# Kernel tuning notes

Hardware: AMD Instinct MI355X
Metric: run time of the kernel (lower is better)

The kernel has to match this reference:

```python
import math
import jax, jax.numpy as jnp
import numpy as np

EMB_DIM = 1024
CFG_N_HEADS = 16
# Faithful to the torch module: n_heads collapses to 1 when config.n_heads < emb_dim
N_HEADS = CFG_N_HEADS if CFG_N_HEADS >= EMB_DIM else 1


def setup_inputs() -> dict:
    key = jax.random.key(0)
    ks = jax.random.split(key, 11)
    B, T, C = 4, 2048, EMB_DIM
    s = 1.0 / math.sqrt(C)
    return {
        "q": jax.random.normal(ks[0], (B, T, C), jnp.float32),
        "k": jax.random.normal(ks[1], (B, T, C), jnp.float32),
        "v": jax.random.normal(ks[2], (B, T, C), jnp.float32),
        "Wq": jax.random.normal(ks[3], (C, C), jnp.float32) * s,
        "bq": jax.random.normal(ks[4], (C,), jnp.float32) * s,
        "Wk": jax.random.normal(ks[5], (C, C), jnp.float32) * s,
        "bk": jax.random.normal(ks[6], (C,), jnp.float32) * s,
        "Wv": jax.random.normal(ks[7], (C, C), jnp.float32) * s,
        "bv": jax.random.normal(ks[8], (C,), jnp.float32) * s,
        "Wff": jax.random.normal(ks[9], (C, C), jnp.float32) * s,
        "bff": jax.random.normal(ks[10], (C,), jnp.float32) * s,
    }


def reference(q, k, v, Wq, bq, Wk, bk, Wv, bv, Wff, bff):
    B, T, C = q.shape
    H = N_HEADS
    D = C // H  # head dim (== C here since H degenerates to 1)
    # torch Linear: x @ W.T + b
    qp = (q @ Wq.T + bq).reshape(B, T, H, D).transpose(0, 2, 1, 3)  # [B,H,T,D]
    kp = (k @ Wk.T + bk).reshape(B, T, H, D).transpose(0, 2, 1, 3)
    vp = (v @ Wv.T + bv).reshape(B, T, H, D).transpose(0, 2, 1, 3)
    scale = 1.0 / math.sqrt(D)
    scores = jnp.einsum('bhqd,bhkd->bhqk', qp, kp) * scale  # [B,H,T,T]
    causal = jnp.tril(jnp.ones((T, T), dtype=bool))
    scores = jnp.where(causal[None, None, :, :], scores, -jnp.inf)
    attn = jax.nn.softmax(scores, axis=-1)
    out = jnp.einsum('bhqk,bhkd->bhqd', attn, vp)  # [B,H,T,D]
    out = out.transpose(0, 2, 1, 3).reshape(B, T, C)
    return out @ Wff.T + bff
```

## Files before the change

kernel.cpp:

```cpp
#include <hip/hip_runtime.h>
#include <stdint.h>

typedef unsigned short u16;
typedef short v8s __attribute__((ext_vector_type(8)));
typedef short s4 __attribute__((ext_vector_type(4)));
typedef float v4f __attribute__((ext_vector_type(4)));

#define BM 128
#define BN 128
#define BK 64

__device__ __forceinline__ float b2f(u16 b) {
  union { unsigned u; float f; } x; x.u = ((unsigned)b) << 16; return x.f;
}
__device__ __forceinline__ u16 f2b(float f) {
  union { float f; unsigned u; } x; x.f = f;
  unsigned r = x.u + 0x7fffu + ((x.u >> 16) & 1u);
  return (u16)(r >> 16);
}

__device__ __forceinline__ void async_copy16(const void* g, void* lds) {
  __builtin_amdgcn_global_load_lds(
      (const __attribute__((address_space(1))) void*)g,
      (__attribute__((address_space(3))) void*)(uint32_t)(uintptr_t)lds,
      16, 0, 0);
}

__device__ __forceinline__ void xcd_swz(int& bx, int& by) {
  const int gx = gridDim.x;
  const int nwg = gx * gridDim.y;
  const int ord = blockIdx.y * gx + blockIdx.x;
  const int q = nwg >> 3, r = nwg & 7;
  const int xcd = ord & 7, local = ord >> 3;
  const int base = xcd < r ? xcd * (q + 1) : r * (q + 1) + (xcd - r) * q;
  const int s = base + local;
  bx = s % gx;
  by = s / gx;
}

__device__ __forceinline__ void causal_pair_swz(int& bx, int& by) {
  const int gx = gridDim.x;
  const int ord = blockIdx.y * gx + blockIdx.x;
  const int k = ord & 7;
  const int j = ord >> 3;
  by = (j < gx) ? k : 15 - k;
  bx = (j < gx) ? j : j - gx;
}

__global__ __launch_bounds__(256) void cvt_all_kernel(
    const float* __restrict__ i0, const float* __restrict__ i1,
    const float* __restrict__ i2, const float* __restrict__ i3,
    const float* __restrict__ i4, const float* __restrict__ i5,
    const float* __restrict__ i6, u16* __restrict__ o0, u16* __restrict__ o1,
    u16* __restrict__ o2, u16* __restrict__ o3, u16* __restrict__ o4,
    u16* __restrict__ o5, u16* __restrict__ o6, u16* __restrict__ o7,
    int n_big, int n_small, int n_l) {
  const int z = blockIdx.y;
  const int i = (blockIdx.x * 256 + threadIdx.x) * 8;
  if (z == 7) {
    if (i < n_l) *(v8s*)(o7 + i) = v8s{0, 0, 0, 0, 0, 0, 0, 0};
    return;
  }
  const float* in;
  u16* out;
  int n;
  switch (z) {
    case 0: in = i0; out = o0; n = n_big; break;
    case 1: in = i1; out = o1; n = n_big; break;
    case 2: in = i2; out = o2; n = n_big; break;
    case 3: in = i3; out = o3; n = n_small; break;
    case 4: in = i4; out = o4; n = n_small; break;
    case 5: in = i5; out = o5; n = n_small; break;
    default: in = i6; out = o6; n = n_small; break;
  }
  if (i >= n) return;
  v4f a = *(const v4f*)(in + i);
  v4f b = *(const v4f*)(in + i + 4);
  v8s o;
#pragma unroll
  for (int j = 0; j < 4; j++) o[j] = (short)f2b(a[j]);
#pragma unroll
  for (int j = 0; j < 4; j++) o[4 + j] = (short)f2b(b[j]);
  *(v8s*)(out + i) = o;
}

struct LdsS { u16 a[BM * BK]; u16 b[BN * BK]; };
union LdsU {
  LdsS s;
  u16 t[128 * 136];
};

template <bool HAS_BIAS, bool CAUSAL_K, bool OUT_F32, bool TR_OUT,
          bool EXP_OUT, bool NORM_L>
__device__ __forceinline__ void gemm_body(
    u16* ldsA, u16* ldsB, u16* ldsT, const u16* __restrict__ A, int lda,
    const u16* __restrict__ Bm, int ldb, void* __restrict__ Cout_, int ldc,
    long cbase, const float* __restrict__ bias, float* __restrict__ lsum,
    int K, int m0, int n0) {
  const int tid = threadIdx.x;
  const int wave = tid >> 6, lane = tid & 63;
  const int wm = (wave >> 1) * 64, wn = (wave & 1) * 64;
  const int lrow = lane & 15, quad = lane >> 4;

  v4f acc[4][4];
#pragma unroll
  for (int i = 0; i < 4; i++)
#pragma unroll
    for (int j = 0; j < 4; j++) acc[i][j] = v4f{0.f, 0.f, 0.f, 0.f};

  int Keff = K;
  if (CAUSAL_K) {
    int ke = m0 + BM;
    Keff = ke < K ? ke : K;
  }

  const int rA = lane >> 3;
  const int uch = (lane & 7) ^ rA;
  const u16* pA = A + (long)(m0 + wave * 8 + rA) * lda + uch * 8;
  const u16* pB = Bm + (long)(n0 + wave * 8 + rA) * ldb + uch * 8;
  u16* dA = ldsA + (wave * 8) * BK;
  u16* dB = ldsB + (wave * 8) * BK;

  for (int k0 = 0; k0 < Keff; k0 += BK) {
#pragma unroll
    for (int c = 0; c < 4; c++) {
      async_copy16(pA + (long)c * 32 * lda + k0, dA + c * 32 * BK);
      async_copy16(pB + (long)c * 32 * ldb + k0, dB + c * 32 * BK);
    }
    __syncthreads();

#pragma unroll
    for (int ks = 0; ks < 2; ks++) {
      v8s af[4], bfr[4];
#pragma unroll
      for (int mt = 0; mt < 4; mt++) {
        const int r = wm + mt * 16 + lrow;
        af[mt] =
            *(const v8s*)&ldsA[r * BK + ((ks * 4 + quad) ^ (r & 7)) * 8];
      }
#pragma unroll
      for (int nt = 0; nt < 4; nt++) {
        const int r = wn + nt * 16 + lrow;
        bfr[nt] =
            *(const v8s*)&ldsB[r * BK + ((ks * 4 + quad) ^ (r & 7)) * 8];
      }
#pragma unroll
      for (int mt = 0; mt < 4; mt++)
#pragma unroll
        for (int nt = 0; nt < 4; nt++)
          acc[mt][nt] = __builtin_amdgcn_mfma_f32_16x16x32_bf16(
              af[mt], bfr[nt], acc[mt][nt], 0, 0, 0);
    }
    __syncthreads();
  }

  if (TR_OUT) {
#pragma unroll
    for (int mt = 0; mt < 4; mt++) {
      const int rl = wm + mt * 16 + quad * 4;
#pragma unroll
      for (int nt = 0; nt < 4; nt++) {
        const int cl = wn + nt * 16 + lrow;
        float bv = 0.f;
        if (HAS_BIAS) bv = bias[n0 + cl];
        s4 w;
#pragma unroll
        for (int i = 0; i < 4; i++) w[i] = (short)f2b(acc[mt][nt][i] + bv);
        *(s4*)&ldsT[cl * 136 + rl] = w;
      }
    }
    __syncthreads();
    const int cl2 = tid >> 1, th = (tid & 1) * 64;
    const long bbase =
        (long)(m0 >> 11) * ((long)1024 * 2048) + (long)(m0 & 2047);
    u16* dst = (u16*)Cout_ + bbase + (long)(n0 + cl2) * 2048 + th;
    const u16* srcl = &ldsT[cl2 * 136 + th];
#pragma unroll
    for (int j = 0; j < 8; j++)
      *(v8s*)(dst + j * 8) = *(const v8s*)(srcl + j * 8);
    return;
  }

  if (EXP_OUT) {
    const float scale = 0.03125f;
#pragma unroll
    for (int mt = 0; mt < 4; mt++) {
      const int rowBase = m0 + wm + mt * 16 + quad * 4;
#pragma unroll
      for (int i = 0; i < 4; i++) {
        const int row = rowBase + i;
        float part = 0.f;
#pragma unroll
        for (int nt = 0; nt < 4; nt++) {
          const int col = n0 + wn + nt * 16 + lrow;
          float e = 0.f;
          if (col <= row) e = __expf(acc[mt][nt][i] * scale);
          part += e;
          ((u16*)Cout_)[cbase + (long)row * ldc + col] = f2b(e);
        }
        part += __shfl_xor(part, 1);
        part += __shfl_xor(part, 2);
        part += __shfl_xor(part, 4);
        part += __shfl_xor(part, 8);
        if (lrow == 0) atomicAdd(&lsum[row], part);
      }
    }
    return;
  }

  if (NORM_L) {
#pragma unroll
    for (int mt = 0; mt < 4; mt++) {
      const int rowBase = m0 + wm + mt * 16 + quad * 4;
#pragma unroll
      for (int i = 0; i < 4; i++) {
        const float inv = 1.0f / lsum[rowBase + i];
#pragma unroll
        for (int nt = 0; nt < 4; nt++) {
          const int col = n0 + wn + nt * 16 + lrow;
          ((u16*)Cout_)[cbase + (long)(rowBase + i) * ldc + col] =
              f2b(acc[mt][nt][i] * inv);
        }
      }
    }
    return;
  }

#pragma unroll
  for (int mt = 0; mt < 4; mt++) {
    const int rowBase = m0 + wm + mt * 16 + quad * 4;
#pragma unroll
    for (int nt = 0; nt < 4; nt++) {
      const int col = n0 + wn + nt * 16 + lrow;
      float bv = 0.f;
      if (HAS_BIAS) bv = bias[col];
#pragma unroll
      for (int i = 0; i < 4; i++) {
        const long idx = cbase + (long)(rowBase + i) * ldc + col;
        const float val = acc[mt][nt][i] + bv;
        if (OUT_F32)
          ((float*)Cout_)[idx] = val;
        else
          ((u16*)Cout_)[idx] = f2b(val);
      }
    }
  }
}

__global__ __launch_bounds__(256, 4) void qkv_gemm_kernel(
    const u16* __restrict__ a0, const u16* __restrict__ a1,
    const u16* __restrict__ a2, const u16* __restrict__ w0,
    const u16* __restrict__ w1, const u16* __restrict__ w2,
    const float* __restrict__ b0, const float* __restrict__ b1,
    const float* __restrict__ b2, u16* __restrict__ c0, u16* __restrict__ c1,
    u16* __restrict__ c2, int C) {
  __shared__ LdsU lds;
  const int z = blockIdx.z;
  const u16* A = z == 0 ? a0 : (z == 1 ? a1 : a2);
  const u16* W = z == 0 ? w0 : (z == 1 ? w1 : w2);
  const float* bias = z == 0 ? b0 : (z == 1 ? b1 : b2);
  u16* Cp = z == 0 ? c0 : (z == 1 ? c1 : c2);
  int bx, by;
  xcd_swz(bx, by);
  if (z == 2)
    gemm_body<true, false, false, true, false, false>(
        lds.s.a, lds.s.b, lds.t, A, C, W, C, Cp, C, 0, bias, nullptr, C,
        by * BM, bx * BN);
  else
    gemm_body<true, false, false, false, false, false>(
        lds.s.a, lds.s.b, nullptr, A, C, W, C, Cp, C, 0, bias, nullptr, C,
        by * BM, bx * BN);
}

template <bool HAS_BIAS, bool CAUSAL_SKIP, bool CAUSAL_K, bool OUT_F32,
          int SWZ, bool EXP_OUT, bool NORM_L>
__global__ __launch_bounds__(256, 4) void gemm_bt_kernel(
    const u16* __restrict__ A, int lda, long sA,
    const u16* __restrict__ Bm, int ldb, long sB,
    void* __restrict__ Cout_, int ldc, long sC,
    const float* __restrict__ bias, float* __restrict__ lsum, int K) {
  __shared__ LdsS lds;
  int bx, by;
  if (SWZ == 1)
    causal_pair_swz(bx, by);
  else
    xcd_swz(bx, by);
  const int m0 = by * BM;
  const int n0 = bx * BN;
  if (CAUSAL_SKIP && n0 > m0) return;
  const int z = blockIdx.z;
  gemm_body<HAS_BIAS, CAUSAL_K, OUT_F32, false, EXP_OUT, NORM_L>(
      lds.a, lds.b, nullptr, A + (long)z * sA, lda, Bm + (long)z * sB, ldb,
      Cout_, ldc, (long)z * sC, bias,
      lsum ? lsum + (long)z * 2048 : nullptr, K, m0, n0);
}

extern "C" void kernel_launch(void* const* d_in, const int* in_sizes, int n_in,
                              void* d_out, int out_size, void* d_ws,
                              size_t ws_size, hipStream_t stream) {
  const float* q = (const float*)d_in[0];
  const float* k = (const float*)d_in[1];
  const float* v = (const float*)d_in[2];
  const float* Wq = (const float*)d_in[3];
  const float* bq = (const float*)d_in[4];
  const float* Wk = (const float*)d_in[5];
  const float* bk = (const float*)d_in[6];
  const float* Wv = (const float*)d_in[7];
  const float* bv = (const float*)d_in[8];
  const float* Wff = (const float*)d_in[9];
  const float* bff = (const float*)d_in[10];
  float* out = (float*)d_out;

  const int B = 4, T = 2048, C = 1024, M = B * T;
  const size_t MC = (size_t)M * C;
  const size_t CC = (size_t)C * C;
  u16* ws = (u16*)d_ws;
  u16* qb = ws;
  u16* kb = qb + MC;
  u16* vb = kb + MC;
  u16* Wqb = vb + MC;
  u16* Wkb = Wqb + CC;
  u16* Wvb = Wkb + CC;
  u16* Wffb = Wvb + CC;
  u16* Qp = Wffb + CC;
  u16* Kp = Qp + MC;
  u16* Vp = Kp + MC;
  u16* VpT = Vp + MC;
  float* lsum = (float*)(VpT + MC);
  u16* S = qb;
  u16* attn = Vp;

  dim3 blk(256);
  cvt_all_kernel<<<dim3((int)(MC / 2048), 8), blk, 0, stream>>>(
      q, k, v, Wq, Wk, Wv, Wff, qb, kb, vb, Wqb, Wkb, Wvb, Wffb,
      (u16*)lsum, (int)MC, (int)CC, B * T * 2);

  qkv_gemm_kernel<<<dim3(C / BN, M / BM, 3), blk, 0, stream>>>(
      qb, kb, vb, Wqb, Wkb, Wvb, bq, bk, bv, Qp, Kp, VpT, C);
  gemm_bt_kernel<false, true, false, false, 1, true, false>
      <<<dim3(T / BN, T / BM, B), blk, 0, stream>>>(
          Qp, C, (long)T * C, Kp, C, (long)T * C, S, T, (long)T * T,
          nullptr, lsum, C);
  gemm_bt_kernel<false, false, true, false, 1, false, true>
      <<<dim3(C / BN, T / BM, B), blk, 0, stream>>>(
          S, T, (long)T * T, VpT, T, (long)C * T, attn, C, (long)T * C,
          nullptr, lsum, T);
  gemm_bt_kernel<true, false, false, true, 0, false, false>
      <<<dim3(C / BN, M / BM, 1), blk, 0, stream>>>(
          attn, C, 0, Wffb, C, 0, out, C, 0, bff, nullptr, C);
}
```

Measured before the change: 318.3 us.

## Fuse fp32-to-bf16 activation conversion into QKV GEMM A-tile loads

The separate conversion pass over the q/k/v activations is removed. The QKV GEMM now reads fp32 A tiles straight from global memory into registers, converts them to bf16 and writes them into swizzled LDS, while the weight tiles still use async global-to-LDS copies. This drops a full write and re-read of three bf16 activation tensors. In exchange, the A loads become synchronous register loads that each block repeats for every N tile, and the A-side load traffic doubles because it is now fp32. The workspace layout is also reshuffled.

Result: slower. 329.3 us (+3.4%).

```diff
diff --git a/kernel.cpp b/kernel.cpp
--- a/kernel.cpp
+++ b/kernel.cpp
@@ -47,31 +47,24 @@
   bx = (j < gx) ? j : j - gx;
 }
 
-__global__ __launch_bounds__(256) void cvt_all_kernel(
+__global__ __launch_bounds__(256) void cvt_w_kernel(
     const float* __restrict__ i0, const float* __restrict__ i1,
     const float* __restrict__ i2, const float* __restrict__ i3,
-    const float* __restrict__ i4, const float* __restrict__ i5,
-    const float* __restrict__ i6, u16* __restrict__ o0, u16* __restrict__ o1,
-    u16* __restrict__ o2, u16* __restrict__ o3, u16* __restrict__ o4,
-    u16* __restrict__ o5, u16* __restrict__ o6, u16* __restrict__ o7,
-    int n_big, int n_small, int n_l) {
+    u16* __restrict__ o0, u16* __restrict__ o1, u16* __restrict__ o2,
+    u16* __restrict__ o3, u16* __restrict__ o4, int n, int n_l) {
   const int z = blockIdx.y;
   const int i = (blockIdx.x * 256 + threadIdx.x) * 8;
-  if (z == 7) {
-    if (i < n_l) *(v8s*)(o7 + i) = v8s{0, 0, 0, 0, 0, 0, 0, 0};
+  if (z == 4) {
+    if (i < n_l) *(v8s*)(o4 + i) = v8s{0, 0, 0, 0, 0, 0, 0, 0};
     return;
   }
   const float* in;
   u16* out;
-  int n;
   switch (z) {
-    case 0: in = i0; out = o0; n = n_big; break;
-    case 1: in = i1; out = o1; n = n_big; break;
-    case 2: in = i2; out = o2; n = n_big; break;
-    case 3: in = i3; out = o3; n = n_small; break;
-    case 4: in = i4; out = o4; n = n_small; break;
-    case 5: in = i5; out = o5; n = n_small; break;
-    default: in = i6; out = o6; n = n_small; break;
+    case 0: in = i0; out = o0; break;
+    case 1: in = i1; out = o1; break;
+    case 2: in = i2; out = o2; break;
+    default: in = i3; out = o3; break;
   }
   if (i >= n) return;
   v4f a = *(const v4f*)(in + i);
@@ -91,9 +84,9 @@
 };
 
 template <bool HAS_BIAS, bool CAUSAL_K, bool OUT_F32, bool TR_OUT,
-          bool EXP_OUT, bool NORM_L>
+          bool EXP_OUT, bool NORM_L, bool A_F32>
 __device__ __forceinline__ void gemm_body(
-    u16* ldsA, u16* ldsB, u16* ldsT, const u16* __restrict__ A, int lda,
+    u16* ldsA, u16* ldsB, u16* ldsT, const void* __restrict__ A, int lda,
     const u16* __restrict__ Bm, int ldb, void* __restrict__ Cout_, int ldc,
     long cbase, const float* __restrict__ bias, float* __restrict__ lsum,
     int K, int m0, int n0) {
@@ -116,16 +109,44 @@
 
   const int rA = lane >> 3;
   const int uch = (lane & 7) ^ rA;
-  const u16* pA = A + (long)(m0 + wave * 8 + rA) * lda + uch * 8;
+  const u16* pA = nullptr;
+  const float* pAf = nullptr;
+  if (A_F32)
+    pAf = (const float*)A + (long)(m0 + wave * 8 + rA) * lda + uch * 8;
+  else
+    pA = (const u16*)A + (long)(m0 + wave * 8 + rA) * lda + uch * 8;
   const u16* pB = Bm + (long)(n0 + wave * 8 + rA) * ldb + uch * 8;
   u16* dA = ldsA + (wave * 8) * BK;
   u16* dB = ldsB + (wave * 8) * BK;
+  u16* wAbase = ldsA + (wave * 8 + rA) * BK + (lane & 7) * 8;
 
   for (int k0 = 0; k0 < Keff; k0 += BK) {
-#pragma unroll
-    for (int c = 0; c < 4; c++) {
-      async_copy16(pA + (long)c * 32 * lda + k0, dA + c * 32 * BK);
-      async_copy16(pB + (long)c * 32 * ldb + k0, dB + c * 32 * BK);
+    if (A_F32) {
+      v4f lo[4], hi[4];
+#pragma unroll
+      for (int c = 0; c < 4; c++) {
+        const float* p = pAf + (long)c * 32 * lda + k0;
+        lo[c] = *(const v4f*)p;
+        hi[c] = *(const v4f*)(p + 4);
+      }
+#pragma unroll
+      for (int c = 0; c < 4; c++)
+        async_copy16(pB + (long)c * 32 * ldb + k0, dB + c * 32 * BK);
+#pragma unroll
+      for (int c = 0; c < 4; c++) {
+        v8s w;
+#pragma unroll
+        for (int j = 0; j < 4; j++) w[j] = (short)f2b(lo[c][j]);
+#pragma unroll
+        for (int j = 0; j < 4; j++) w[4 + j] = (short)f2b(hi[c][j]);
+        *(v8s*)(wAbase + c * 32 * BK) = w;
+      }
+    } else {
+#pragma unroll
+      for (int c = 0; c < 4; c++) {
+        async_copy16(pA + (long)c * 32 * lda + k0, dA + c * 32 * BK);
+        async_copy16(pB + (long)c * 32 * ldb + k0, dB + c * 32 * BK);
+      }
     }
     __syncthreads();
 
@@ -248,26 +269,26 @@
 }
 
 __global__ __launch_bounds__(256, 4) void qkv_gemm_kernel(
-    const u16* __restrict__ a0, const u16* __restrict__ a1,
-    const u16* __restrict__ a2, const u16* __restrict__ w0,
+    const float* __restrict__ a0, const float* __restrict__ a1,
+    const float* __restrict__ a2, const u16* __restrict__ w0,
     const u16* __restrict__ w1, const u16* __restrict__ w2,
     const float* __restrict__ b0, const float* __restrict__ b1,
     const float* __restrict__ b2, u16* __restrict__ c0, u16* __restrict__ c1,
     u16* __restrict__ c2, int C) {
   __shared__ LdsU lds;
   const int z = blockIdx.z;
-  const u16* A = z == 0 ? a0 : (z == 1 ? a1 : a2);
+  const float* A = z == 0 ? a0 : (z == 1 ? a1 : a2);
   const u16* W = z == 0 ? w0 : (z == 1 ? w1 : w2);
   const float* bias = z == 0 ? b0 : (z == 1 ? b1 : b2);
   u16* Cp = z == 0 ? c0 : (z == 1 ? c1 : c2);
   int bx, by;
   xcd_swz(bx, by);
   if (z == 2)
-    gemm_body<true, false, false, true, false, false>(
+    gemm_body<true, false, false, true, false, false, true>(
         lds.s.a, lds.s.b, lds.t, A, C, W, C, Cp, C, 0, bias, nullptr, C,
         by * BM, bx * BN);
   else
-    gemm_body<true, false, false, false, false, false>(
+    gemm_body<true, false, false, false, false, false, true>(
         lds.s.a, lds.s.b, nullptr, A, C, W, C, Cp, C, 0, bias, nullptr, C,
         by * BM, bx * BN);
 }
@@ -289,7 +310,7 @@
   const int n0 = bx * BN;
   if (CAUSAL_SKIP && n0 > m0) return;
   const int z = blockIdx.z;
-  gemm_body<HAS_BIAS, CAUSAL_K, OUT_F32, false, EXP_OUT, NORM_L>(
+  gemm_body<HAS_BIAS, CAUSAL_K, OUT_F32, false, EXP_OUT, NORM_L, false>(
       lds.a, lds.b, nullptr, A + (long)z * sA, lda, Bm + (long)z * sB, ldb,
       Cout_, ldc, (long)z * sC, bias,
       lsum ? lsum + (long)z * 2048 : nullptr, K, m0, n0);
@@ -315,28 +336,23 @@
   const size_t MC = (size_t)M * C;
   const size_t CC = (size_t)C * C;
   u16* ws = (u16*)d_ws;
-  u16* qb = ws;
-  u16* kb = qb + MC;
-  u16* vb = kb + MC;
-  u16* Wqb = vb + MC;
+  u16* Wqb = ws;
   u16* Wkb = Wqb + CC;
   u16* Wvb = Wkb + CC;
   u16* Wffb = Wvb + CC;
   u16* Qp = Wffb + CC;
   u16* Kp = Qp + MC;
-  u16* Vp = Kp + MC;
-  u16* VpT = Vp + MC;
-  float* lsum = (float*)(VpT + MC);
-  u16* S = qb;
-  u16* attn = Vp;
+  u16* VpT = Kp + MC;
+  u16* attn = VpT + MC;
+  u16* S = attn + MC;
+  float* lsum = (float*)(S + 2 * MC);
 
   dim3 blk(256);
-  cvt_all_kernel<<<dim3((int)(MC / 2048), 8), blk, 0, stream>>>(
-      q, k, v, Wq, Wk, Wv, Wff, qb, kb, vb, Wqb, Wkb, Wvb, Wffb,
-      (u16*)lsum, (int)MC, (int)CC, B * T * 2);
+  cvt_w_kernel<<<dim3((int)(CC / 2048), 5), blk, 0, stream>>>(
+      Wq, Wk, Wv, Wff, Wqb, Wkb, Wvb, Wffb, (u16*)lsum, (int)CC, B * T * 2);
 
   qkv_gemm_kernel<<<dim3(C / BN, M / BM, 3), blk, 0, stream>>>(
-      qb, kb, vb, Wqb, Wkb, Wvb, bq, bk, bv, Qp, Kp, VpT, C);
+      q, k, v, Wqb, Wkb, Wvb, bq, bk, bv, Qp, Kp, VpT, C);
   gemm_bt_kernel<false, true, false, false, 1, true, false>
       <<<dim3(T / BN, T / BM, B), blk, 0, stream>>>(
           Qp, C, (long)T * C, Kp, C, (long)T * C, S, T, (long)T * T,
```
